# Kernel optimization log

Hardware: AMD Instinct MI355X
Metric: run time of the kernel (lower is better)

## Reference

```python
import jax, jax.numpy as jnp
import numpy as np

NUM_TRAIN = 256  # num_train_anchors
N, A, T = 8, 131072, 64


def _make_boxes(key, shape2):
    # shape2 = (..., 2) of (y, x); returns valid boxes (y1, x1, y2, x2) in [0, 1]
    k1, k2 = jax.random.split(key)
    c1 = jax.random.uniform(k1, shape2, dtype=jnp.float32)
    c2 = jax.random.uniform(k2, shape2, dtype=jnp.float32)
    lo = jnp.minimum(c1, c2)
    hi = jnp.maximum(c1, c2)
    return jnp.stack([lo[..., 0], lo[..., 1], hi[..., 0], hi[..., 1]], axis=-1)


def setup_inputs() -> dict:
    key = jax.random.key(0)
    ka, kt, kp, kn = jax.random.split(key, 4)
    return {
        "anchors": _make_boxes(ka, (N, A, 2)),
        "true_bboxes": _make_boxes(kt, (N, T, 2)),
        "rand_pos": jax.random.uniform(kp, (N, A), dtype=jnp.float32),
        "rand_neg": jax.random.uniform(kn, (N, A), dtype=jnp.float32),
    }


def _bbox_overlap(anchors, gt):
    # anchors [A,4], gt [T,4] -> IoU [A,T]
    ay1, ax1, ay2, ax2 = [anchors[:, i] for i in range(4)]
    gy1, gx1, gy2, gx2 = [gt[:, i] for i in range(4)]
    a_area = (ay2 - ay1) * (ax2 - ax1)                       # [A]
    g_area = (gy2 - gy1) * (gx2 - gx1)                       # [T]
    ih = jnp.clip(jnp.minimum(ay2[:, None], gy2[None, :]) - jnp.maximum(ay1[:, None], gy1[None, :]), 0.0)
    iw = jnp.clip(jnp.minimum(ax2[:, None], gx2[None, :]) - jnp.maximum(ax1[:, None], gx1[None, :]), 0.0)
    inter = ih * iw                                          # [A,T]
    union = a_area[:, None] + g_area[None, :] - inter
    return jnp.where(union > 0, inter / jnp.where(union > 0, union, 1.0), 0.0)


def _rank_of(scores):
    # rank[i] = position of element i in ascending sort of scores
    order = jnp.argsort(scores)
    return jnp.zeros(scores.shape[0], jnp.int32).at[order].set(jnp.arange(scores.shape[0], dtype=jnp.int32))


def _compute_bbox_deltas(anchors, gt):
    # standard (dy, dx, dh, dw) encoding with safe denominators
    ah = anchors[:, 2] - anchors[:, 0]
    aw = anchors[:, 3] - anchors[:, 1]
    acy = anchors[:, 0] + 0.5 * ah
    acx = anchors[:, 1] + 0.5 * aw
    gh = gt[:, 2] - gt[:, 0]
    gw = gt[:, 3] - gt[:, 1]
    gcy = gt[:, 0] + 0.5 * gh
    gcx = gt[:, 1] + 0.5 * gw
    ah_s = jnp.where(ah > 0, ah, 1.0)
    aw_s = jnp.where(aw > 0, aw, 1.0)
    gh_s = jnp.where(gh > 0, gh, 1.0)
    gw_s = jnp.where(gw > 0, gw, 1.0)
    return jnp.stack([(gcy - acy) / ah_s, (gcx - acx) / aw_s,
                      jnp.log(gh_s / ah_s), jnp.log(gw_s / aw_s)], axis=-1)


def _get_targets(anchors, gt, r_pos, r_neg):
    na = anchors.shape[0]
    # strip_out_of_bounds_anchors: zero out anchors falling outside [0,1]^2 (keeps static shape)
    inb = (anchors[:, 0] >= 0) & (anchors[:, 1] >= 0) & (anchors[:, 2] <= 1) & (anchors[:, 3] <= 1)
    anchors = jnp.where(inb[:, None], anchors, 0.0)

    overlaps = _bbox_overlap(anchors, gt)                    # [A,T]

    # --- class assignment ---
    iou_max_val = jnp.max(overlaps, axis=1)                  # [A]
    classes = jnp.full((na,), -1, jnp.int32)
    classes = jnp.where(iou_max_val < 0.3, 0, classes)
    iou_max_anchor = jnp.argmax(overlaps, axis=0)            # [T] best anchor per gt
    pos_anchor = jnp.zeros((na,), jnp.int32).at[iou_max_anchor].set(1)
    classes = jnp.where(pos_anchor > 0, 1, classes)
    classes = jnp.where(iou_max_val >= 0.7, 1, classes)

    # --- subsample positives to NUM_TRAIN//2 (uniform random subset) ---
    pos = classes > 0
    rank_p = _rank_of(jnp.where(pos, r_pos, jnp.inf))
    keep_pos = pos & (rank_p < NUM_TRAIN // 2)
    classes = jnp.where(pos & ~keep_pos, -1, classes)
    n_pos = jnp.sum(keep_pos.astype(jnp.int32))

    # --- subsample negatives to NUM_TRAIN - n_pos ---
    desired_neg = NUM_TRAIN - n_pos
    neg = classes == 0
    rank_n = _rank_of(jnp.where(neg, r_neg, jnp.inf))
    keep_neg = neg & (rank_n < desired_neg)
    classes = jnp.where(neg & ~keep_neg, -1, classes)

    # --- deltas for positive anchors ---
    best_gt = jnp.argmax(overlaps, axis=1)                   # [A]
    deltas = _compute_bbox_deltas(anchors, gt[best_gt])      # [A,4]
    deltas = jnp.where((classes > 0)[:, None], deltas, 0.0)
    return classes, deltas


def reference(anchors, true_bboxes, rand_pos, rand_neg):
    classes, deltas = jax.vmap(_get_targets)(anchors, true_bboxes, rand_pos, rand_neg)
    return classes, deltas
```

## Files before the change

kernel.cpp:

```cpp
#include <hip/hip_runtime.h>
#include <stdint.h>

#define N_B 8
#define A_N 131072
#define T_N 64
#define NUM_TRAIN 256
#define NEG_TAU 0.05f
#define ITEM_CAP 512
#define HSET 512
#define APT 2
#define SEG_A 512
#define GBLK_A 256
#define CAPP 128
#define BLK_C 128
#define SEG_C 1024

typedef unsigned long long u64;
typedef unsigned int u32;

__device__ __forceinline__ float iou_one(float ay1, float ax1, float ay2, float ax2,
                                         float a_area, float gy1, float gx1, float gy2,
                                         float gx2, float g_area) {
#pragma clang fp contract(off)
    float ih = fmaxf(fminf(ay2, gy2) - fmaxf(ay1, gy1), 0.0f);
    float iw = fmaxf(fminf(ax2, gx2) - fmaxf(ax1, gx1), 0.0f);
    float inter = ih * iw;
    float uni = (a_area + g_area) - inter;
    return uni > 0.0f ? inter / uni : 0.0f;
}

__global__ void __launch_bounds__(256) k_main(const float4* __restrict__ anchors4,
                                              const float4* __restrict__ gts4,
                                              const float* __restrict__ rpos,
                                              const float* __restrict__ rneg,
                                              unsigned char* __restrict__ preclass,
                                              long long* __restrict__ colpack,
                                              u64* __restrict__ pos_list,
                                              u64* __restrict__ neg_list,
                                              int* __restrict__ bcp, int* __restrict__ bcn,
                                              int* __restrict__ hist_pos,
                                              int* __restrict__ hist_neg) {
    __shared__ float4 gbox[T_N];
    __shared__ float gars[T_N];
    __shared__ u64 cmax[T_N];
    __shared__ int lcnt[2];
    int n = blockIdx.y, bx = blockIdx.x, tid = threadIdx.x, lane = tid & 63;
    int a0 = bx * SEG_A + tid;
    size_t nA = (size_t)n * A_N;

    if (tid < T_N) {
        float4 gb = gts4[n * T_N + tid];
        gbox[tid] = gb;
        {
#pragma clang fp contract(off)
            gars[tid] = (gb.z - gb.x) * (gb.w - gb.y);
        }
        cmax[tid] = 0;
    }
    if (tid < 2) lcnt[tid] = 0;
    __syncthreads();

    float ay1[APT], ax1[APT], ay2[APT], ax2[APT], aar[APT], vmax[APT];
#pragma unroll
    for (int k = 0; k < APT; k++) {
        float4 ab = anchors4[nA + a0 + k * 256];
        float y1 = ab.x, x1 = ab.y, y2 = ab.z, x2 = ab.w;
        bool inb = (y1 >= 0.f) && (x1 >= 0.f) && (y2 <= 1.f) && (x2 <= 1.f);
        if (!inb) { y1 = x1 = y2 = x2 = 0.f; }
        ay1[k] = y1; ax1[k] = x1; ay2[k] = y2; ax2[k] = x2;
        {
#pragma clang fp contract(off)
            aar[k] = (y2 - y1) * (x2 - x1);
        }
        vmax[k] = 0.f;
    }

#pragma unroll 4
    for (int jj = 0; jj < T_N; jj++) {
        int j = (lane + jj) & (T_N - 1);
        float4 gb = gbox[j];
        float gar = gars[j];
        float vb = iou_one(ay1[0], ax1[0], ay2[0], ax2[0], aar[0], gb.x, gb.y, gb.z, gb.w, gar);
        vmax[0] = fmaxf(vmax[0], vb);
        int kb = 0;
#pragma unroll
        for (int k = 1; k < APT; k++) {
            float v = iou_one(ay1[k], ax1[k], ay2[k], ax2[k], aar[k], gb.x, gb.y, gb.z, gb.w, gar);
            vmax[k] = fmaxf(vmax[k], v);
            if (v > vb) { vb = v; kb = k; }
        }
        u64 pk = ((u64)__float_as_uint(vb) << 32) | (u32)(~(u32)(a0 + (kb << 8)));
        atomicMax(&cmax[j], pk);
    }

    size_t segbase = ((size_t)(n * GBLK_A + bx)) << 7;
#pragma unroll
    for (int k = 0; k < APT; k++) {
        int a = a0 + k * 256;
        float vm = vmax[k];
        int c0 = (vm < 0.3f) ? 0 : ((vm >= 0.7f) ? 1 : -1);
        preclass[nA + a] = (unsigned char)(signed char)c0;
        if (c0 == 1) {
            int sl = atomicAdd(&lcnt[0], 1);
            if (sl < CAPP) {
                float r = rpos[nA + a];
                pos_list[segbase + sl] = ((u64)__float_as_uint(r) << 32) | (u32)a;
                int bb = (int)(r * 256.0f); bb = bb > 255 ? 255 : bb;
                atomicAdd(&hist_pos[(n << 8) + bb], 1);
            }
        } else if (c0 == 0) {
            float r = rneg[nA + a];
            if (r < NEG_TAU) {
                int sl = atomicAdd(&lcnt[1], 1);
                if (sl < CAPP) {
                    neg_list[segbase + sl] = ((u64)__float_as_uint(r) << 32) | (u32)a;
                    int bb = (int)(r * (256.0f / NEG_TAU)); bb = bb > 255 ? 255 : bb;
                    atomicAdd(&hist_neg[(n << 8) + bb], 1);
                }
            }
        }
    }
    __syncthreads();
    if (tid < T_N) atomicMax(&colpack[(n << 6) + tid], (long long)cmax[tid]);
    if (tid == 0) {
        bcp[n * GBLK_A + bx] = lcnt[0] < CAPP ? lcnt[0] : CAPP;
        bcn[n * GBLK_A + bx] = lcnt[1] < CAPP ? lcnt[1] : CAPP;
    }
}

__device__ __forceinline__ bool in_hset(const int* hset, int a) {
    u32 h = ((u32)a * 2654435761u) >> 23 & (HSET - 1);
    while (true) {
        int v = hset[h];
        if (v == -1) return false;
        if (v == a) return true;
        h = (h + 1) & (HSET - 1);
    }
}

__device__ u64 tail_select(const u64* lists, const int* cnts,
                           const u64* extras, int ecnt, const int* hset, bool use_excl,
                           int k, float scale, u64 ovf_all,
                           int* hist, u64* items, int* misc, int* wsum, u64* result) {
    int tid = threadIdx.x, lane = tid & 63, wid = tid >> 6;
    if (tid == 0) { misc[0] = 0; *result = ovf_all; }
    __syncthreads();

    int h = hist[tid], v = h;
#pragma unroll
    for (int d = 1; d < 64; d <<= 1) {
        int t = __shfl_up(v, d, 64);
        if (lane >= d) v += t;
    }
    if (lane == 63) wsum[wid] = v;
    __syncthreads();
    int total = wsum[0] + wsum[1] + wsum[2] + wsum[3];
    int base = 0;
    for (int w = 0; w < wid; w++) base += wsum[w];
    int incl = base + v, exc = incl - h;
    if (k >= exc && k < incl) { misc[1] = tid; misc[2] = exc; }
    if (tid == 0) misc[3] = total;
    __syncthreads();
    if (k >= total) return ovf_all;
    int b = misc[1], before = misc[2];

    int c = cnts[tid];
    const ulonglong2* b2 = (const ulonglong2*)(lists + ((size_t)tid << 7));
    int nch = (c + 1) >> 1;
    {
        ulonglong2 q;
        if (nch > 0) q = b2[0];
        for (int ci = 0; ci < nch; ci++) {
            ulonglong2 qn;
            if (ci + 1 < nch) qn = b2[ci + 1];
            {
                u64 p = q.x; int a = (int)(u32)p;
                if (!use_excl || !in_hset(hset, a)) {
                    float vv = __uint_as_float((u32)(p >> 32));
                    int bn = (int)(vv * scale); bn = bn > 255 ? 255 : bn;
                    if (bn == b) { int ix = atomicAdd(&misc[0], 1); if (ix < ITEM_CAP) items[ix] = p; }
                }
            }
            if (2 * ci + 1 < c) {
                u64 p = q.y; int a = (int)(u32)p;
                if (!use_excl || !in_hset(hset, a)) {
                    float vv = __uint_as_float((u32)(p >> 32));
                    int bn = (int)(vv * scale); bn = bn > 255 ? 255 : bn;
                    if (bn == b) { int ix = atomicAdd(&misc[0], 1); if (ix < ITEM_CAP) items[ix] = p; }
                }
            }
            q = qn;
        }
    }
    for (int i = tid; i < ecnt; i += 256) {
        u64 p = extras[i];
        float vv = __uint_as_float((u32)(p >> 32));
        int bn = (int)(vv * scale); bn = bn > 255 ? 255 : bn;
        if (bn == b) { int ix = atomicAdd(&misc[0], 1); if (ix < ITEM_CAP) items[ix] = p; }
    }
    __syncthreads();
    int m = misc[0]; m = m < ITEM_CAP ? m : ITEM_CAP;
    int target = k - before;
    for (int i = tid; i < m; i += 256) {
        u64 p = items[i];
        int r = 0;
        for (int j = 0; j < m; j++) r += (items[j] < p);
        if (r == target) *result = p;
    }
    __syncthreads();
    u64 res = *result;
    __syncthreads();
    return res;
}

__global__ void __launch_bounds__(256) k_C(const float4* __restrict__ anchors4,
                                           const float4* __restrict__ gts4,
                                           const u32* __restrict__ preclass32,
                                           const unsigned char* __restrict__ preclass,
                                           const long long* __restrict__ colpack,
                                           const u64* __restrict__ pos_list,
                                           const u64* __restrict__ neg_list,
                                           const int* __restrict__ bcp,
                                           const int* __restrict__ bcn,
                                           const int* __restrict__ hist_pos_g,
                                           const int* __restrict__ hist_neg_g,
                                           const float* __restrict__ rpos,
                                           const float4* __restrict__ rpos4,
                                           const float4* __restrict__ rneg4,
                                           float4* __restrict__ out_classes4,
                                           float4* __restrict__ out_deltas) {
    __shared__ float4 gbox[T_N];
    __shared__ float gars[T_N];
    __shared__ u32 wbm[32];
    __shared__ u32 pbm[32];
    __shared__ int hist[256];
    __shared__ u64 items[ITEM_CAP];
    __shared__ int hset[HSET];
    __shared__ u64 extras[T_N];
    __shared__ int wnrs[T_N];
    __shared__ int misc[4];
    __shared__ int wsum[4];
    __shared__ int shr[4];
    __shared__ u64 result;
    int n = blockIdx.y, bx = blockIdx.x, tid = threadIdx.x;
    size_t nA = (size_t)n * A_N;

    if (tid < 32) { wbm[tid] = 0; pbm[tid] = 0; }
    for (int i = tid; i < HSET; i += 256) hset[i] = -1;
    hist[tid] = hist_pos_g[(n << 8) + tid];
    if (tid < T_N) {
        float4 gb = gts4[n * T_N + tid];
        gbox[tid] = gb;
        {
#pragma clang fp contract(off)
            gars[tid] = (gb.z - gb.x) * (gb.w - gb.y);
        }
    }
    __syncthreads();

    int w = 0, pcv = 0;
    bool dup = false;
    if (tid < T_N) {
        u64 m = (u64)colpack[(n << 6) + tid];
        w = (int)(~(u32)(m & 0xFFFFFFFFull));
        wnrs[tid] = w;
        int d = w - bx * SEG_C;
        if ((u32)d < (u32)SEG_C) atomicOr(&wbm[d >> 5], 1u << (d & 31));
        u32 hh = ((u32)w * 2654435761u) >> 23 & (HSET - 1);
        while (true) {
            int old = atomicCAS(&hset[hh], -1, w);
            if (old == -1 || old == w) break;
            hh = (hh + 1) & (HSET - 1);
        }
    }
    __syncthreads();
    if (tid < T_N) {
        for (int t2 = 0; t2 < tid; t2++) dup |= (wnrs[t2] == w);
        pcv = (int)(signed char)preclass[nA + w];
        bool val = !dup && (pcv != 1);
        u64 mask = __ballot(val);
        if (val) {
            int ix = (int)__popcll(mask & ((1ull << tid) - 1));
            extras[ix] = ((u64)__float_as_uint(rpos[nA + w]) << 32) | (u32)w;
        }
        if (tid == 0) shr[0] = (int)__popcll(mask);
    }
    __syncthreads();
    int extra_cnt = shr[0];
    for (int i = tid; i < extra_cnt; i += 256) {
        float vv = __uint_as_float((u32)(extras[i] >> 32));
        int bb = (int)(vv * 256.0f); bb = bb > 255 ? 255 : bb;
        atomicAdd(&hist[bb], 1);
    }
    __syncthreads();

    u64 cp = tail_select(pos_list + (((size_t)n * GBLK_A) << 7), bcp + n * GBLK_A,
                         extras, extra_cnt, hset, false,
                         NUM_TRAIN / 2, 256.0f, ~0ull,
                         hist, items, misc, wsum, &result);
    int P = misc[3];

    hist[tid] = hist_neg_g[(n << 8) + tid];
    __syncthreads();
    if (tid < T_N && !dup && pcv == 0) {
        float r = __uint_as_float((u32)0);
        (void)r;
    }
    if (tid < T_N && !dup && pcv == 0) {
        float r = rneg4[(nA + (size_t)w) / 4].x;
        const float* rn = (const float*)rneg4;
        r = rn[nA + w];
        if (r < NEG_TAU) {
            int bb = (int)(r * (256.0f / NEG_TAU)); bb = bb > 255 ? 255 : bb;
            atomicAdd(&hist[bb], -1);
        }
    }
    __syncthreads();
    int n_pos = P < NUM_TRAIN / 2 ? P : NUM_TRAIN / 2;
    u64 cn = tail_select(neg_list + (((size_t)n * GBLK_A) << 7), bcn + n * GBLK_A,
                         nullptr, 0, hset, true,
                         NUM_TRAIN - n_pos, 256.0f / NEG_TAU,
                         ((u64)__float_as_uint(NEG_TAU) << 32),
                         hist, items, misc, wsum, &result);

    size_t gi4 = nA / 4 + bx * 256 + tid;
    u32 pcw = preclass32[gi4];
    float4 rp = rpos4[gi4];
    float4 rn = rneg4[gi4];
    float rpv[4] = {rp.x, rp.y, rp.z, rp.w};
    float rnv[4] = {rn.x, rn.y, rn.z, rn.w};
    int a0 = (bx * 256 + tid) * 4;

    u32 marked = (wbm[tid >> 3] >> ((tid & 7) * 4)) & 0xF;

    float fcv[4];
#pragma unroll
    for (int j = 0; j < 4; j++) {
        int c = (int)(signed char)((pcw >> (8 * j)) & 0xFF);
        if ((marked >> j) & 1) c = 1;
        int a = a0 + j;
        int fc = -1;
        if (c == 1) {
            u64 p = ((u64)__float_as_uint(rpv[j]) << 32) | (u32)a;
            fc = (p < cp) ? 1 : -1;
        } else if (c == 0) {
            u64 p = ((u64)__float_as_uint(rnv[j]) << 32) | (u32)a;
            fc = (p < cn) ? 0 : -1;
        }
        fcv[j] = (float)fc;
        if (fc == 1) {
            int s = 4 * tid + j;
            atomicOr(&pbm[s >> 5], 1u << (s & 31));
        }
    }
    out_classes4[gi4] = make_float4(fcv[0], fcv[1], fcv[2], fcv[3]);
    __syncthreads();

    int base = bx * SEG_C;
#pragma unroll
    for (int j = 0; j < 4; j++) {
        int s = j * 256 + tid;
        float4 d = make_float4(0.f, 0.f, 0.f, 0.f);
        if ((pbm[s >> 5] >> (s & 31)) & 1) {
            int a = base + s;
            float4 ab = anchors4[nA + a];
            float ay1 = ab.x, ax1 = ab.y, ay2 = ab.z, ax2 = ab.w;
            bool inb = (ay1 >= 0.f) && (ax1 >= 0.f) && (ay2 <= 1.f) && (ax2 <= 1.f);
            if (!inb) { ay1 = ax1 = ay2 = ax2 = 0.f; }
            float a_area;
            {
#pragma clang fp contract(off)
                a_area = (ay2 - ay1) * (ax2 - ax1);
            }
            float vm = 0.f; int jb = 0;
            for (int t = 0; t < T_N; t++) {
                float4 gb = gbox[t];
                float v = iou_one(ay1, ax1, ay2, ax2, a_area, gb.x, gb.y, gb.z, gb.w, gars[t]);
                bool g = v > vm;
                vm = g ? v : vm;
                jb = g ? t : jb;
            }
            float4 gb = gbox[jb];
            float ah = ay2 - ay1, aw = ax2 - ax1;
            float acy = ay1 + 0.5f * ah, acx = ax1 + 0.5f * aw;
            float gh = gb.z - gb.x, gw = gb.w - gb.y;
            float gcy = gb.x + 0.5f * gh, gcx = gb.y + 0.5f * gw;
            float ah_s = ah > 0.f ? ah : 1.f, aw_s = aw > 0.f ? aw : 1.f;
            float gh_s = gh > 0.f ? gh : 1.f, gw_s = gw > 0.f ? gw : 1.f;
            d.x = (gcy - acy) / ah_s;
            d.y = (gcx - acx) / aw_s;
            d.z = logf(gh_s / ah_s);
            d.w = logf(gw_s / aw_s);
        }
        out_deltas[nA + base + s] = d;
    }
}

extern "C" void kernel_launch(void* const* d_in, const int* in_sizes, int n_in,
                              void* d_out, int out_size, void* d_ws, size_t ws_size,
                              hipStream_t stream) {
    const float4* anchors4 = (const float4*)d_in[0];
    const float4* gts4     = (const float4*)d_in[1];
    const float*  rpos     = (const float*)d_in[2];
    const float*  rneg     = (const float*)d_in[3];

    char* p = (char*)d_ws;
    long long* colpack = (long long*)p; p += N_B * T_N * sizeof(long long);
    u64* pos_list = (u64*)p;  p += (size_t)N_B * GBLK_A * CAPP * sizeof(u64);
    u64* neg_list = (u64*)p;  p += (size_t)N_B * GBLK_A * CAPP * sizeof(u64);
    unsigned char* preclass = (unsigned char*)p; p += (size_t)N_B * A_N;
    int* bcp  = (int*)p;  p += N_B * GBLK_A * sizeof(int);
    int* bcn  = (int*)p;  p += N_B * GBLK_A * sizeof(int);
    int* hist_pos_g = (int*)p; p += N_B * 256 * sizeof(int);
    int* hist_neg_g = (int*)p; p += N_B * 256 * sizeof(int);

    float4* out_classes4 = (float4*)d_out;
    float4* out_deltas   = (float4*)((float*)d_out + (size_t)N_B * A_N);

    hipMemsetAsync(hist_pos_g, 0, 2 * N_B * 256 * sizeof(int), stream);

    k_main<<<dim3(GBLK_A, N_B), 256, 0, stream>>>(anchors4, gts4, rpos, rneg, preclass,
                                                  colpack, pos_list, neg_list, bcp, bcn,
                                                  hist_pos_g, hist_neg_g);
    k_C<<<dim3(BLK_C, N_B), 256, 0, stream>>>(anchors4, gts4, (const u32*)preclass, preclass,
                                              colpack, pos_list, neg_list, bcp, bcn,
                                              hist_pos_g, hist_neg_g, rpos,
                                              (const float4*)rpos, (const float4*)rneg,
                                              out_classes4, out_deltas);
}
```

Before: 190.1 us.

## Fuse main and finalize kernels via last-block election and spin-wait on cutoffs

Merges the IoU/preclassification kernel and the selection/output kernel into one launch. The last block to finish per image runs the tail-select and publishes the cutoffs, while the other blocks spin-wait on them and then write classes and deltas from values still held in registers. The preclass buffer goes away, the winner's preclass is packed into colpack, and rpos, rneg and the anchors are not reloaded. The spin-wait assumes every block of the grid is co-resident (2048 blocks at 8 per CU), otherwise it can deadlock. It also serialises each image's tail-select behind all of that image's blocks.

```diff
diff --git a/kernel.cpp b/kernel.cpp
--- a/kernel.cpp
+++ b/kernel.cpp
@@ -12,11 +12,22 @@
 #define SEG_A 512
 #define GBLK_A 256
 #define CAPP 128
-#define BLK_C 128
-#define SEG_C 1024
 
 typedef unsigned long long u64;
 typedef unsigned int u32;
+
+__device__ __forceinline__ u64 aload64(const u64* p) {
+    return __hip_atomic_load((u64*)p, __ATOMIC_RELAXED, __HIP_MEMORY_SCOPE_AGENT);
+}
+__device__ __forceinline__ int aload32(const int* p) {
+    return __hip_atomic_load((int*)p, __ATOMIC_RELAXED, __HIP_MEMORY_SCOPE_AGENT);
+}
+__device__ __forceinline__ void astore64(u64* p, u64 v) {
+    __hip_atomic_store(p, v, __ATOMIC_RELAXED, __HIP_MEMORY_SCOPE_AGENT);
+}
+__device__ __forceinline__ void astore32(int* p, int v) {
+    __hip_atomic_store(p, v, __ATOMIC_RELAXED, __HIP_MEMORY_SCOPE_AGENT);
+}
 
 __device__ __forceinline__ float iou_one(float ay1, float ax1, float ay2, float ax2,
                                          float a_area, float gy1, float gx1, float gy2,
@@ -29,21 +40,110 @@
     return uni > 0.0f ? inter / uni : 0.0f;
 }
 
-__global__ void __launch_bounds__(256) k_main(const float4* __restrict__ anchors4,
-                                              const float4* __restrict__ gts4,
-                                              const float* __restrict__ rpos,
-                                              const float* __restrict__ rneg,
-                                              unsigned char* __restrict__ preclass,
-                                              long long* __restrict__ colpack,
-                                              u64* __restrict__ pos_list,
-                                              u64* __restrict__ neg_list,
-                                              int* __restrict__ bcp, int* __restrict__ bcn,
-                                              int* __restrict__ hist_pos,
-                                              int* __restrict__ hist_neg) {
+__device__ __forceinline__ bool in_hset(const int* hset, int a) {
+    u32 h = ((u32)a * 2654435761u) >> 23 & (HSET - 1);
+    while (true) {
+        int v = hset[h];
+        if (v == -1) return false;
+        if (v == a) return true;
+        h = (h + 1) & (HSET - 1);
+    }
+}
+
+__device__ u64 tail_select(const u64* list, const int* cnts,
+                           const u64* extras, int ecnt, const int* hset, bool use_excl,
+                           int k, float scale, u64 ovf_all,
+                           int* hist, u64* items, int* misc, int* wsum, u64* result) {
+    int tid = threadIdx.x, lane = tid & 63, wid = tid >> 6;
+    if (tid == 0) { misc[0] = 0; *result = ovf_all; }
+    __syncthreads();
+
+    int h = hist[tid], v = h;
+#pragma unroll
+    for (int d = 1; d < 64; d <<= 1) {
+        int t = __shfl_up(v, d, 64);
+        if (lane >= d) v += t;
+    }
+    if (lane == 63) wsum[wid] = v;
+    __syncthreads();
+    int total = wsum[0] + wsum[1] + wsum[2] + wsum[3];
+    int base = 0;
+    for (int w = 0; w < wid; w++) base += wsum[w];
+    int incl = base + v, exc = incl - h;
+    if (k >= exc && k < incl) { misc[1] = tid; misc[2] = exc; }
+    if (tid == 0) misc[3] = total;
+    __syncthreads();
+    if (k >= total) return ovf_all;
+    int b = misc[1], before = misc[2];
+
+#define PROC(P) do { u64 p_ = (P); int a_ = (int)(u32)p_;                                   \
+        if (!use_excl || !in_hset(hset, a_)) {                                              \
+            float v_ = __uint_as_float((u32)(p_ >> 32));                                    \
+            int bn_ = (int)(v_ * scale); bn_ = bn_ > 255 ? 255 : bn_;                       \
+            if (bn_ == b) { int ix_ = atomicAdd(&misc[0], 1);                               \
+                            if (ix_ < ITEM_CAP) items[ix_] = p_; } } } while (0)
+
+    int c = aload32(&cnts[tid]);
+    const u64* lp = list + ((size_t)tid << 7);
+    for (int ci = 0; ci < c; ci += 4) {
+        u64 p0 = aload64(&lp[ci]);
+        u64 p1 = (ci + 1 < c) ? aload64(&lp[ci + 1]) : 0;
+        u64 p2 = (ci + 2 < c) ? aload64(&lp[ci + 2]) : 0;
+        u64 p3 = (ci + 3 < c) ? aload64(&lp[ci + 3]) : 0;
+        PROC(p0);
+        if (ci + 1 < c) PROC(p1);
+        if (ci + 2 < c) PROC(p2);
+        if (ci + 3 < c) PROC(p3);
+    }
+    for (int i = tid; i < ecnt; i += 256) PROC(extras[i]);
+#undef PROC
+    __syncthreads();
+    int m = misc[0]; m = m < ITEM_CAP ? m : ITEM_CAP;
+    int target = k - before;
+    for (int i = tid; i < m; i += 256) {
+        u64 p = items[i];
+        int r = 0;
+        for (int j = 0; j < m; j++) r += (items[j] < p);
+        if (r == target) *result = p;
+    }
+    __syncthreads();
+    u64 res = *result;
+    __syncthreads();
+    return res;
+}
+
+__global__ void __launch_bounds__(256, 8) k_fused(const float4* __restrict__ anchors4,
+                                                  const float4* __restrict__ gts4,
+                                                  const float* __restrict__ rpos,
+                                                  const float* __restrict__ rneg,
+                                                  long long* __restrict__ colpack,
+                                                  u64* __restrict__ pos_list,
+                                                  u64* __restrict__ neg_list,
+                                                  int* __restrict__ bcp, int* __restrict__ bcn,
+                                                  int* __restrict__ hist_pos,
+                                                  int* __restrict__ hist_neg,
+                                                  int* __restrict__ done_cnt,
+                                                  u64* __restrict__ cutoff,
+                                                  float* __restrict__ out_classes,
+                                                  float4* __restrict__ out_deltas) {
     __shared__ float4 gbox[T_N];
     __shared__ float gars[T_N];
     __shared__ u64 cmax[T_N];
     __shared__ int lcnt[2];
+    __shared__ signed char c0s[SEG_A];
+    __shared__ u32 wbm[16];
+    __shared__ int hist[256];
+    __shared__ u64 items[ITEM_CAP];
+    __shared__ int hset[HSET];
+    __shared__ u64 extras[T_N];
+    __shared__ int wnrs[T_N];
+    __shared__ int misc[4];
+    __shared__ int wsum[4];
+    __shared__ int shr[4];
+    __shared__ u64 result;
+    __shared__ u64 scut[2];
+    __shared__ int slast;
+
     int n = blockIdx.y, bx = blockIdx.x, tid = threadIdx.x, lane = tid & 63;
     int a0 = bx * SEG_A + tid;
     size_t nA = (size_t)n * A_N;
@@ -58,6 +158,7 @@
         cmax[tid] = 0;
     }
     if (tid < 2) lcnt[tid] = 0;
+    if (tid < 16) wbm[tid] = 0;
     __syncthreads();
 
     float ay1[APT], ax1[APT], ay2[APT], ax2[APT], aar[APT], vmax[APT];
@@ -93,296 +194,171 @@
         atomicMax(&cmax[j], pk);
     }
 
+    int myc0[APT];
+    float myrp[APT], myrn[APT];
     size_t segbase = ((size_t)(n * GBLK_A + bx)) << 7;
 #pragma unroll
     for (int k = 0; k < APT; k++) {
         int a = a0 + k * 256;
         float vm = vmax[k];
         int c0 = (vm < 0.3f) ? 0 : ((vm >= 0.7f) ? 1 : -1);
-        preclass[nA + a] = (unsigned char)(signed char)c0;
+        myc0[k] = c0;
+        c0s[tid + k * 256] = (signed char)c0;
+        float rp = rpos[nA + a], rn = rneg[nA + a];
+        myrp[k] = rp; myrn[k] = rn;
         if (c0 == 1) {
             int sl = atomicAdd(&lcnt[0], 1);
             if (sl < CAPP) {
-                float r = rpos[nA + a];
-                pos_list[segbase + sl] = ((u64)__float_as_uint(r) << 32) | (u32)a;
-                int bb = (int)(r * 256.0f); bb = bb > 255 ? 255 : bb;
+                astore64(&pos_list[segbase + sl], ((u64)__float_as_uint(rp) << 32) | (u32)a);
+                int bb = (int)(rp * 256.0f); bb = bb > 255 ? 255 : bb;
                 atomicAdd(&hist_pos[(n << 8) + bb], 1);
             }
         } else if (c0 == 0) {
-            float r = rneg[nA + a];
-            if (r < NEG_TAU) {
+            if (rn < NEG_TAU) {
                 int sl = atomicAdd(&lcnt[1], 1);
                 if (sl < CAPP) {
-                    neg_list[segbase + sl] = ((u64)__float_as_uint(r) << 32) | (u32)a;
-                    int bb = (int)(r * (256.0f / NEG_TAU)); bb = bb > 255 ? 255 : bb;
+                    astore64(&neg_list[segbase + sl], ((u64)__float_as_uint(rn) << 32) | (u32)a);
+                    int bb = (int)(rn * (256.0f / NEG_TAU)); bb = bb > 255 ? 255 : bb;
                     atomicAdd(&hist_neg[(n << 8) + bb], 1);
                 }
             }
         }
     }
     __syncthreads();
-    if (tid < T_N) atomicMax(&colpack[(n << 6) + tid], (long long)cmax[tid]);
+
+    if (tid < T_N) {
+        u64 m = cmax[tid];
+        u32 wg = ~(u32)m;
+        int wl = (int)wg - bx * SEG_A;
+        u32 enc = (u32)c0s[wl] & 3u;
+        u64 pk = (m & 0xFFFFFFFF00000000ull) | (u32)(~((wg << 2) | enc));
+        atomicMax(&colpack[(n << 6) + tid], (long long)pk);
+    }
     if (tid == 0) {
-        bcp[n * GBLK_A + bx] = lcnt[0] < CAPP ? lcnt[0] : CAPP;
-        bcn[n * GBLK_A + bx] = lcnt[1] < CAPP ? lcnt[1] : CAPP;
-    }
-}
-
-__device__ __forceinline__ bool in_hset(const int* hset, int a) {
-    u32 h = ((u32)a * 2654435761u) >> 23 & (HSET - 1);
-    while (true) {
-        int v = hset[h];
-        if (v == -1) return false;
-        if (v == a) return true;
-        h = (h + 1) & (HSET - 1);
-    }
-}
-
-__device__ u64 tail_select(const u64* lists, const int* cnts,
-                           const u64* extras, int ecnt, const int* hset, bool use_excl,
-                           int k, float scale, u64 ovf_all,
-                           int* hist, u64* items, int* misc, int* wsum, u64* result) {
-    int tid = threadIdx.x, lane = tid & 63, wid = tid >> 6;
-    if (tid == 0) { misc[0] = 0; *result = ovf_all; }
-    __syncthreads();
-
-    int h = hist[tid], v = h;
+        astore32(&bcp[n * GBLK_A + bx], lcnt[0] < CAPP ? lcnt[0] : CAPP);
+        astore32(&bcn[n * GBLK_A + bx], lcnt[1] < CAPP ? lcnt[1] : CAPP);
+    }
+
+    asm volatile("s_waitcnt vmcnt(0) lgkmcnt(0)" ::: "memory");
+    __syncthreads();
+    if (tid == 0) slast = (atomicAdd(&done_cnt[n], 1) == GBLK_A - 1) ? 1 : 0;
+    __syncthreads();
+
+    if (slast) {
+        for (int i = tid; i < HSET; i += 256) hset[i] = -1;
+        hist[tid] = aload32(&hist_pos[(n << 8) + tid]);
+        __syncthreads();
+
+        int w = 0, pcv = 0;
+        bool dup = false;
+        if (tid < T_N) {
+            u64 m = aload64((const u64*)&colpack[(n << 6) + tid]);
+            u32 ie = ~(u32)m;
+            w = (int)(ie >> 2);
+            pcv = ((ie & 3u) == 3u) ? -1 : (int)(ie & 3u);
+            wnrs[tid] = w;
+            u32 hh = ((u32)w * 2654435761u) >> 23 & (HSET - 1);
+            while (true) {
+                int old = atomicCAS(&hset[hh], -1, w);
+                if (old == -1 || old == w) break;
+                hh = (hh + 1) & (HSET - 1);
+            }
+        }
+        __syncthreads();
+        if (tid < T_N) {
+            for (int t2 = 0; t2 < tid; t2++) dup |= (wnrs[t2] == w);
+            bool val = !dup && (pcv != 1);
+            u64 mask = __ballot(val);
+            if (val) {
+                int ix = (int)__popcll(mask & ((1ull << tid) - 1));
+                extras[ix] = ((u64)__float_as_uint(rpos[nA + w]) << 32) | (u32)w;
+            }
+            if (tid == 0) shr[0] = (int)__popcll(mask);
+        }
+        __syncthreads();
+        int extra_cnt = shr[0];
+        for (int i = tid; i < extra_cnt; i += 256) {
+            float vv = __uint_as_float((u32)(extras[i] >> 32));
+            int bb = (int)(vv * 256.0f); bb = bb > 255 ? 255 : bb;
+            atomicAdd(&hist[bb], 1);
+        }
+        __syncthreads();
+
+        u64 cp = tail_select(pos_list + (((size_t)n * GBLK_A) << 7), bcp + n * GBLK_A,
+                             extras, extra_cnt, hset, false,
+                             NUM_TRAIN / 2, 256.0f, ~0ull,
+                             hist, items, misc, wsum, &result);
+        int P = misc[3];
+
+        hist[tid] = aload32(&hist_neg[(n << 8) + tid]);
+        __syncthreads();
+        if (tid < T_N && !dup && pcv == 0) {
+            float r = rneg[nA + w];
+            if (r < NEG_TAU) {
+                int bb = (int)(r * (256.0f / NEG_TAU)); bb = bb > 255 ? 255 : bb;
+                atomicAdd(&hist[bb], -1);
+            }
+        }
+        __syncthreads();
+        int n_pos = P < NUM_TRAIN / 2 ? P : NUM_TRAIN / 2;
+        u64 cn = tail_select(neg_list + (((size_t)n * GBLK_A) << 7), bcn + n * GBLK_A,
+                             nullptr, 0, hset, true,
+                             NUM_TRAIN - n_pos, 256.0f / NEG_TAU,
+                             ((u64)__float_as_uint(NEG_TAU) << 32),
+                             hist, items, misc, wsum, &result);
+        if (tid == 0) {
+            astore64(&cutoff[2 * n], cp);
+            astore64(&cutoff[2 * n + 1], cn);
+            scut[0] = cp; scut[1] = cn;
+        }
+    } else if (tid == 0) {
+        u64 v;
+        do { v = aload64(&cutoff[2 * n]); if (v != 0) break; __builtin_amdgcn_s_sleep(8); } while (true);
+        scut[0] = v;
+        do { v = aload64(&cutoff[2 * n + 1]); if (v != 0) break; __builtin_amdgcn_s_sleep(2); } while (true);
+        scut[1] = v;
+    }
+    __syncthreads();
+    u64 cp = scut[0], cn = scut[1];
+
+    if (tid < T_N) {
+        u64 m = aload64((const u64*)&colpack[(n << 6) + tid]);
+        int w = (int)((~(u32)m) >> 2);
+        int d = w - bx * SEG_A;
+        if ((u32)d < (u32)SEG_A) atomicOr(&wbm[d >> 5], 1u << (d & 31));
+    }
+    __syncthreads();
+
 #pragma unroll
-    for (int d = 1; d < 64; d <<= 1) {
-        int t = __shfl_up(v, d, 64);
-        if (lane >= d) v += t;
-    }
-    if (lane == 63) wsum[wid] = v;
-    __syncthreads();
-    int total = wsum[0] + wsum[1] + wsum[2] + wsum[3];
-    int base = 0;
-    for (int w = 0; w < wid; w++) base += wsum[w];
-    int incl = base + v, exc = incl - h;
-    if (k >= exc && k < incl) { misc[1] = tid; misc[2] = exc; }
-    if (tid == 0) misc[3] = total;
-    __syncthreads();
-    if (k >= total) return ovf_all;
-    int b = misc[1], before = misc[2];
-
-    int c = cnts[tid];
-    const ulonglong2* b2 = (const ulonglong2*)(lists + ((size_t)tid << 7));
-    int nch = (c + 1) >> 1;
-    {
-        ulonglong2 q;
-        if (nch > 0) q = b2[0];
-        for (int ci = 0; ci < nch; ci++) {
-            ulonglong2 qn;
-            if (ci + 1 < nch) qn = b2[ci + 1];
-            {
-                u64 p = q.x; int a = (int)(u32)p;
-                if (!use_excl || !in_hset(hset, a)) {
-                    float vv = __uint_as_float((u32)(p >> 32));
-                    int bn = (int)(vv * scale); bn = bn > 255 ? 255 : bn;
-                    if (bn == b) { int ix = atomicAdd(&misc[0], 1); if (ix < ITEM_CAP) items[ix] = p; }
-                }
-            }
-            if (2 * ci + 1 < c) {
-                u64 p = q.y; int a = (int)(u32)p;
-                if (!use_excl || !in_hset(hset, a)) {
-                    float vv = __uint_as_float((u32)(p >> 32));
-                    int bn = (int)(vv * scale); bn = bn > 255 ? 255 : bn;
-                    if (bn == b) { int ix = atomicAdd(&misc[0], 1); if (ix < ITEM_CAP) items[ix] = p; }
-                }
-            }
-            q = qn;
-        }
-    }
-    for (int i = tid; i < ecnt; i += 256) {
-        u64 p = extras[i];
-        float vv = __uint_as_float((u32)(p >> 32));
-        int bn = (int)(vv * scale); bn = bn > 255 ? 255 : bn;
-        if (bn == b) { int ix = atomicAdd(&misc[0], 1); if (ix < ITEM_CAP) items[ix] = p; }
-    }
-    __syncthreads();
-    int m = misc[0]; m = m < ITEM_CAP ? m : ITEM_CAP;
-    int target = k - before;
-    for (int i = tid; i < m; i += 256) {
-        u64 p = items[i];
-        int r = 0;
-        for (int j = 0; j < m; j++) r += (items[j] < p);
-        if (r == target) *result = p;
-    }
-    __syncthreads();
-    u64 res = *result;
-    __syncthreads();
-    return res;
-}
-
-__global__ void __launch_bounds__(256) k_C(const float4* __restrict__ anchors4,
-                                           const float4* __restrict__ gts4,
-                                           const u32* __restrict__ preclass32,
-                                           const unsigned char* __restrict__ preclass,
-                                           const long long* __restrict__ colpack,
-                                           const u64* __restrict__ pos_list,
-                                           const u64* __restrict__ neg_list,
-                                           const int* __restrict__ bcp,
-                                           const int* __restrict__ bcn,
-                                           const int* __restrict__ hist_pos_g,
-                                           const int* __restrict__ hist_neg_g,
-                                           const float* __restrict__ rpos,
-                                           const float4* __restrict__ rpos4,
-                                           const float4* __restrict__ rneg4,
-                                           float4* __restrict__ out_classes4,
-                                           float4* __restrict__ out_deltas) {
-    __shared__ float4 gbox[T_N];
-    __shared__ float gars[T_N];
-    __shared__ u32 wbm[32];
-    __shared__ u32 pbm[32];
-    __shared__ int hist[256];
-    __shared__ u64 items[ITEM_CAP];
-    __shared__ int hset[HSET];
-    __shared__ u64 extras[T_N];
-    __shared__ int wnrs[T_N];
-    __shared__ int misc[4];
-    __shared__ int wsum[4];
-    __shared__ int shr[4];
-    __shared__ u64 result;
-    int n = blockIdx.y, bx = blockIdx.x, tid = threadIdx.x;
-    size_t nA = (size_t)n * A_N;
-
-    if (tid < 32) { wbm[tid] = 0; pbm[tid] = 0; }
-    for (int i = tid; i < HSET; i += 256) hset[i] = -1;
-    hist[tid] = hist_pos_g[(n << 8) + tid];
-    if (tid < T_N) {
-        float4 gb = gts4[n * T_N + tid];
-        gbox[tid] = gb;
-        {
-#pragma clang fp contract(off)
-            gars[tid] = (gb.z - gb.x) * (gb.w - gb.y);
-        }
-    }
-    __syncthreads();
-
-    int w = 0, pcv = 0;
-    bool dup = false;
-    if (tid < T_N) {
-        u64 m = (u64)colpack[(n << 6) + tid];
-        w = (int)(~(u32)(m & 0xFFFFFFFFull));
-        wnrs[tid] = w;
-        int d = w - bx * SEG_C;
-        if ((u32)d < (u32)SEG_C) atomicOr(&wbm[d >> 5], 1u << (d & 31));
-        u32 hh = ((u32)w * 2654435761u) >> 23 & (HSET - 1);
-        while (true) {
-            int old = atomicCAS(&hset[hh], -1, w);
-            if (old == -1 || old == w) break;
-            hh = (hh + 1) & (HSET - 1);
-        }
-    }
-    __syncthreads();
-    if (tid < T_N) {
-        for (int t2 = 0; t2 < tid; t2++) dup |= (wnrs[t2] == w);
-        pcv = (int)(signed char)preclass[nA + w];
-        bool val = !dup && (pcv != 1);
-        u64 mask = __ballot(val);
-        if (val) {
-            int ix = (int)__popcll(mask & ((1ull << tid) - 1));
-            extras[ix] = ((u64)__float_as_uint(rpos[nA + w]) << 32) | (u32)w;
-        }
-        if (tid == 0) shr[0] = (int)__popcll(mask);
-    }
-    __syncthreads();
-    int extra_cnt = shr[0];
-    for (int i = tid; i < extra_cnt; i += 256) {
-        float vv = __uint_as_float((u32)(extras[i] >> 32));
-        int bb = (int)(vv * 256.0f); bb = bb > 255 ? 255 : bb;
-        atomicAdd(&hist[bb], 1);
-    }
-    __syncthreads();
-
-    u64 cp = tail_select(pos_list + (((size_t)n * GBLK_A) << 7), bcp + n * GBLK_A,
-                         extras, extra_cnt, hset, false,
-                         NUM_TRAIN / 2, 256.0f, ~0ull,
-                         hist, items, misc, wsum, &result);
-    int P = misc[3];
-
-    hist[tid] = hist_neg_g[(n << 8) + tid];
-    __syncthreads();
-    if (tid < T_N && !dup && pcv == 0) {
-        float r = __uint_as_float((u32)0);
-        (void)r;
-    }
-    if (tid < T_N && !dup && pcv == 0) {
-        float r = rneg4[(nA + (size_t)w) / 4].x;
-        const float* rn = (const float*)rneg4;
-        r = rn[nA + w];
-        if (r < NEG_TAU) {
-            int bb = (int)(r * (256.0f / NEG_TAU)); bb = bb > 255 ? 255 : bb;
-            atomicAdd(&hist[bb], -1);
-        }
-    }
-    __syncthreads();
-    int n_pos = P < NUM_TRAIN / 2 ? P : NUM_TRAIN / 2;
-    u64 cn = tail_select(neg_list + (((size_t)n * GBLK_A) << 7), bcn + n * GBLK_A,
-                         nullptr, 0, hset, true,
-                         NUM_TRAIN - n_pos, 256.0f / NEG_TAU,
-                         ((u64)__float_as_uint(NEG_TAU) << 32),
-                         hist, items, misc, wsum, &result);
-
-    size_t gi4 = nA / 4 + bx * 256 + tid;
-    u32 pcw = preclass32[gi4];
-    float4 rp = rpos4[gi4];
-    float4 rn = rneg4[gi4];
-    float rpv[4] = {rp.x, rp.y, rp.z, rp.w};
-    float rnv[4] = {rn.x, rn.y, rn.z, rn.w};
-    int a0 = (bx * 256 + tid) * 4;
-
-    u32 marked = (wbm[tid >> 3] >> ((tid & 7) * 4)) & 0xF;
-
-    float fcv[4];
-#pragma unroll
-    for (int j = 0; j < 4; j++) {
-        int c = (int)(signed char)((pcw >> (8 * j)) & 0xFF);
-        if ((marked >> j) & 1) c = 1;
-        int a = a0 + j;
+    for (int k = 0; k < APT; k++) {
+        int l = tid + k * 256;
+        int a = a0 + k * 256;
+        int c = myc0[k];
+        if ((wbm[l >> 5] >> (l & 31)) & 1) c = 1;
         int fc = -1;
         if (c == 1) {
-            u64 p = ((u64)__float_as_uint(rpv[j]) << 32) | (u32)a;
+            u64 p = ((u64)__float_as_uint(myrp[k]) << 32) | (u32)a;
             fc = (p < cp) ? 1 : -1;
         } else if (c == 0) {
-            u64 p = ((u64)__float_as_uint(rnv[j]) << 32) | (u32)a;
+            u64 p = ((u64)__float_as_uint(myrn[k]) << 32) | (u32)a;
             fc = (p < cn) ? 0 : -1;
         }
-        fcv[j] = (float)fc;
+        out_classes[nA + a] = (float)fc;
+
+        float4 d = make_float4(0.f, 0.f, 0.f, 0.f);
         if (fc == 1) {
-            int s = 4 * tid + j;
-            atomicOr(&pbm[s >> 5], 1u << (s & 31));
-        }
-    }
-    out_classes4[gi4] = make_float4(fcv[0], fcv[1], fcv[2], fcv[3]);
-    __syncthreads();
-
-    int base = bx * SEG_C;
-#pragma unroll
-    for (int j = 0; j < 4; j++) {
-        int s = j * 256 + tid;
-        float4 d = make_float4(0.f, 0.f, 0.f, 0.f);
-        if ((pbm[s >> 5] >> (s & 31)) & 1) {
-            int a = base + s;
-            float4 ab = anchors4[nA + a];
-            float ay1 = ab.x, ax1 = ab.y, ay2 = ab.z, ax2 = ab.w;
-            bool inb = (ay1 >= 0.f) && (ax1 >= 0.f) && (ay2 <= 1.f) && (ax2 <= 1.f);
-            if (!inb) { ay1 = ax1 = ay2 = ax2 = 0.f; }
-            float a_area;
-            {
-#pragma clang fp contract(off)
-                a_area = (ay2 - ay1) * (ax2 - ax1);
-            }
             float vm = 0.f; int jb = 0;
             for (int t = 0; t < T_N; t++) {
                 float4 gb = gbox[t];
-                float v = iou_one(ay1, ax1, ay2, ax2, a_area, gb.x, gb.y, gb.z, gb.w, gars[t]);
+                float v = iou_one(ay1[k], ax1[k], ay2[k], ax2[k], aar[k],
+                                  gb.x, gb.y, gb.z, gb.w, gars[t]);
                 bool g = v > vm;
                 vm = g ? v : vm;
                 jb = g ? t : jb;
             }
             float4 gb = gbox[jb];
-            float ah = ay2 - ay1, aw = ax2 - ax1;
-            float acy = ay1 + 0.5f * ah, acx = ax1 + 0.5f * aw;
+            float ah = ay2[k] - ay1[k], aw = ax2[k] - ax1[k];
+            float acy = ay1[k] + 0.5f * ah, acx = ax1[k] + 0.5f * aw;
             float gh = gb.z - gb.x, gw = gb.w - gb.y;
             float gcy = gb.x + 0.5f * gh, gcx = gb.y + 0.5f * gw;
             float ah_s = ah > 0.f ? ah : 1.f, aw_s = aw > 0.f ? aw : 1.f;
@@ -392,7 +368,7 @@
             d.z = logf(gh_s / ah_s);
             d.w = logf(gw_s / aw_s);
         }
-        out_deltas[nA + base + s] = d;
+        out_deltas[nA + a] = d;
     }
 }
 
@@ -405,26 +381,24 @@
     const float*  rneg     = (const float*)d_in[3];
 
     char* p = (char*)d_ws;
+    u64* cutoff     = (u64*)p; p += 2 * N_B * sizeof(u64);
+    int* hist_pos_g = (int*)p; p += N_B * 256 * sizeof(int);
+    int* hist_neg_g = (int*)p; p += N_B * 256 * sizeof(int);
+    int* done_cnt   = (int*)p; p += N_B * sizeof(int);
     long long* colpack = (long long*)p; p += N_B * T_N * sizeof(long long);
     u64* pos_list = (u64*)p;  p += (size_t)N_B * GBLK_A * CAPP * sizeof(u64);
     u64* neg_list = (u64*)p;  p += (size_t)N_B * GBLK_A * CAPP * sizeof(u64);
-    unsigned char* preclass = (unsigned char*)p; p += (size_t)N_B * A_N;
     int* bcp  = (int*)p;  p += N_B * GBLK_A * sizeof(int);
     int* bcn  = (int*)p;  p += N_B * GBLK_A * sizeof(int);
-    int* hist_pos_g = (int*)p; p += N_B * 256 * sizeof(int);
-    int* hist_neg_g = (int*)p; p += N_B * 256 * sizeof(int);
-
-    float4* out_classes4 = (float4*)d_out;
-    float4* out_deltas   = (float4*)((float*)d_out + (size_t)N_B * A_N);
-
-    hipMemsetAsync(hist_pos_g, 0, 2 * N_B * 256 * sizeof(int), stream);
-
-    k_main<<<dim3(GBLK_A, N_B), 256, 0, stream>>>(anchors4, gts4, rpos, rneg, preclass,
-                                                  colpack, pos_list, neg_list, bcp, bcn,
-                                                  hist_pos_g, hist_neg_g);
-    k_C<<<dim3(BLK_C, N_B), 256, 0, stream>>>(anchors4, gts4, (const u32*)preclass, preclass,
-                                              colpack, pos_list, neg_list, bcp, bcn,
-                                              hist_pos_g, hist_neg_g, rpos,
-                                              (const float4*)rpos, (const float4*)rneg,
-                                              out_classes4, out_deltas);
-}
+
+    float* out_classes = (float*)d_out;
+    float4* out_deltas = (float4*)((float*)d_out + (size_t)N_B * A_N);
+
+    size_t zbytes = 2 * N_B * sizeof(u64) + (2 * N_B * 256 + N_B) * sizeof(int);
+    hipMemsetAsync(cutoff, 0, zbytes, stream);
+
+    k_fused<<<dim3(GBLK_A, N_B), 256, 0, stream>>>(anchors4, gts4, rpos, rneg,
+                                                   colpack, pos_list, neg_list, bcp, bcn,
+                                                   hist_pos_g, hist_neg_g, done_cnt, cutoff,
+                                                   out_classes, out_deltas);
+}
```

Measured after the change: 184.1 us. 1.03x faster.
